# Optimization experiments

Hardware: AMD Instinct MI355X
Metric: run time of the kernel (lower is better)

The kernel has to match this reference:

```python
import jax, jax.numpy as jnp
import numpy as np

B, P, N, E, F, L = 64, 512, 512, 128, 512, 6
SQRT_E = 11.313708498984761
CLIP = 10.0
EPS = 1e-5

def _inorm(x, w, b):
    # InstanceNorm1d over node dim (axis=1) per (batch, channel); x: [B,N,E]
    mu = x.mean(axis=1, keepdims=True)
    var = x.var(axis=1, keepdims=True)
    return (x - mu) * jax.lax.rsqrt(var + EPS) * w + b

def setup_inputs():
    key = jax.random.key(0)
    ks = jax.random.split(key, 24)
    nrm = lambda k, shp, s=0.05: jax.random.normal(k, shp, dtype=jnp.float32) * s
    inp = {}
    inp['data'] = jax.random.uniform(ks[0], (B, N, 2), dtype=jnp.float32)
    inp['dist'] = -jax.random.uniform(ks[1], (B, N, N), dtype=jnp.float32)      # negative dist
    inp['cur_dist'] = -jax.random.uniform(ks[2], (B, P, N), dtype=jnp.float32)
    inp['capacity'] = jax.random.uniform(ks[3], (B, P), dtype=jnp.float32)
    inp['ninf_mask'] = jnp.zeros((B, P, N), jnp.float32)
    inp['log_scale'] = jnp.array([1.0], jnp.float32)
    # encoder params (Linear weights stored [in,out], i.e. torch weight transposed)
    inp['emb_W'] = nrm(ks[4], (2, E), 0.5); inp['emb_b'] = jnp.zeros((E,), jnp.float32)
    inp['Wq'] = nrm(ks[5], (L, E, E)); inp['Wk'] = nrm(ks[6], (L, E, E)); inp['Wv'] = nrm(ks[7], (L, E, E))
    inp['aft_alpha'] = jnp.ones((L,), jnp.float32)
    inp['n1_w'] = jnp.ones((L, E), jnp.float32); inp['n1_b'] = jnp.zeros((L, E), jnp.float32)
    inp['ff_W1'] = nrm(ks[8], (L, E, F)); inp['ff_b1'] = jnp.zeros((L, F), jnp.float32)
    inp['ff_W2'] = nrm(ks[9], (L, F, E)); inp['ff_b2'] = jnp.zeros((L, E), jnp.float32)
    inp['n2_w'] = jnp.ones((L, E), jnp.float32); inp['n2_b'] = jnp.zeros((L, E), jnp.float32)
    # decoder params
    inp['dWq'] = nrm(ks[10], (E + 1, E)); inp['dWk'] = nrm(ks[11], (E, E)); inp['dWv'] = nrm(ks[12], (E, E))
    inp['dec_aft_alpha'] = jnp.array([1.0], jnp.float32)
    inp['probs_alpha'] = jnp.array([1.0], jnp.float32)
    return inp

def reference(data, dist, cur_dist, capacity, ninf_mask, log_scale,
              emb_W, emb_b, Wq, Wk, Wv, aft_alpha, n1_w, n1_b,
              ff_W1, ff_b1, ff_W2, ff_b2, n2_w, n2_b,
              dWq, dWk, dWv, dec_aft_alpha, probs_alpha):
    ls = log_scale[0]
    # ---- encoder: stacked AFT layers ----
    x = data @ emb_W + emb_b                                   # [B,N,E]
    for l in range(L):
        q = x @ Wq[l]; k = x @ Wk[l]; v = x @ Wv[l]
        ad = jnp.exp(ls * aft_alpha[l] * dist)                 # [B,N,N]
        ek = jnp.exp(k)
        weighted = (ad @ (ek * v)) / (ad @ ek)                 # [B,N,E]
        out = jax.nn.sigmoid(q) * weighted
        h = _inorm(x + out, n1_w[l], n1_b[l])
        ff = jax.nn.relu(h @ ff_W1[l] + ff_b1[l]) @ ff_W2[l] + ff_b2[l]
        x = _inorm(h + ff, n2_w[l], n2_b[l])
    enc = x                                                    # [B,N,E]
    # ---- decoder ----
    k = enc @ dWk; v = enc @ dWv
    gmean = enc.mean(axis=1, keepdims=True)                    # [B,1,E]
    gmp = jnp.broadcast_to(gmean, (enc.shape[0], capacity.shape[1], enc.shape[2]))
    q = jnp.concatenate([gmp, capacity[:, :, None]], axis=2) @ dWq   # [B,P,E]
    ad = jnp.exp(ls * dec_aft_alpha[0] * cur_dist + ninf_mask)       # [B,P,N]
    ek = jnp.exp(k)
    weighted = (ad @ (ek * v)) / (ad @ ek)                     # [B,P,E]
    aft = jax.nn.sigmoid(q) * weighted
    score = jnp.einsum('bpe,bne->bpn', aft, enc) / SQRT_E
    score = score + ls * probs_alpha[0] * cur_dist
    score = CLIP * jnp.tanh(score) + ninf_mask
    return jax.nn.softmax(score, axis=2)                       # [B,P,N]
```

## Files before the change

### kernel.cpp

```cpp
#include <hip/hip_runtime.h>
#include <math.h>

#define B_ 64
#define N_ 512
#define P_ 512
#define E_ 128
#define F_ 512
#define L_ 6
#define SQRT_E_INV 0.08838834764831843f

typedef unsigned short u16;
typedef __attribute__((ext_vector_type(8))) short bf8;
typedef __attribute__((ext_vector_type(16))) float f16v;

__device__ inline u16 bf16r(float f) {
    unsigned u = __float_as_uint(f);
    u += 0x7fffu + ((u >> 16) & 1u);
    return (u16)(u >> 16);
}
__device__ inline float bf2f(u16 h) { return __uint_as_float((unsigned)h << 16); }

#define MFMA(a, b, c) __builtin_amdgcn_mfma_f32_32x32x16_bf16(a, b, c, 0, 0, 0)

struct Q3 {
    const u16 *A0, *A1;
    const u16 *qh, *ql, *vh, *vl, *kh, *kl;
    u16 *sq16, *y2t;
};

__launch_bounds__(256, 2) __global__ void qvk3_k(Q3 p)
{
    const int tid = threadIdx.x;
    const int lane = tid & 63, wv = tid >> 6;
    const int wm = wv & 1, wn = wv >> 1;
    const int ln = lane & 31, hk = lane >> 5;
    const int row0 = blockIdx.x * 64;

    __shared__ __align__(16) u16 As[2][64][40];
    __shared__ __align__(16) u16 Bs[6][128][40];

    f16v aq[2], av[2], ak[2];
#pragma unroll
    for (int nt = 0; nt < 2; ++nt)
#pragma unroll
        for (int q = 0; q < 16; ++q) { aq[nt][q] = 0.f; av[nt][q] = 0.f; ak[nt][q] = 0.f; }

    const int r = tid >> 2, kq = tid & 3;
    for (int k0 = 0; k0 < 128; k0 += 32) {
        size_t ga = (size_t)(row0 + r) * 128 + k0 + kq * 8;
        *(uint4*)&As[0][r][kq * 8] = *(const uint4*)(p.A0 + ga);
        *(uint4*)&As[1][r][kq * 8] = *(const uint4*)(p.A1 + ga);
#pragma unroll
        for (int i = 0; i < 2; ++i) {
            int s = tid + i * 256;
            int rb2 = s >> 2, q = s & 3;
            size_t gb = (size_t)rb2 * 128 + k0 + q * 8;
            *(uint4*)&Bs[0][rb2][q * 8] = *(const uint4*)(p.qh + gb);
            *(uint4*)&Bs[1][rb2][q * 8] = *(const uint4*)(p.ql + gb);
            *(uint4*)&Bs[2][rb2][q * 8] = *(const uint4*)(p.vh + gb);
            *(uint4*)&Bs[3][rb2][q * 8] = *(const uint4*)(p.vl + gb);
            *(uint4*)&Bs[4][rb2][q * 8] = *(const uint4*)(p.kh + gb);
            *(uint4*)&Bs[5][rb2][q * 8] = *(const uint4*)(p.kl + gb);
        }
        __syncthreads();
#pragma unroll
        for (int s = 0; s < 2; ++s) {
            bf8 ah = *(const bf8*)&As[0][wm * 32 + ln][s * 16 + hk * 8];
            bf8 al = *(const bf8*)&As[1][wm * 32 + ln][s * 16 + hk * 8];
#pragma unroll
            for (int nt = 0; nt < 2; ++nt) {
                const int br = wn * 64 + nt * 32 + ln, sc = s * 16 + hk * 8;
                bf8 bqh = *(const bf8*)&Bs[0][br][sc];
                bf8 bql = *(const bf8*)&Bs[1][br][sc];
                bf8 bvh = *(const bf8*)&Bs[2][br][sc];
                bf8 bvl = *(const bf8*)&Bs[3][br][sc];
                bf8 bkh = *(const bf8*)&Bs[4][br][sc];
                bf8 bkl = *(const bf8*)&Bs[5][br][sc];
                aq[nt] = MFMA(ah, bqh, aq[nt]);
                aq[nt] = MFMA(ah, bql, aq[nt]);
                aq[nt] = MFMA(al, bqh, aq[nt]);
                av[nt] = MFMA(ah, bvh, av[nt]);
                av[nt] = MFMA(ah, bvl, av[nt]);
                av[nt] = MFMA(al, bvh, av[nt]);
                ak[nt] = MFMA(ah, bkh, ak[nt]);
                ak[nt] = MFMA(ah, bkl, ak[nt]);
                ak[nt] = MFMA(al, bkh, ak[nt]);
            }
        }
        __syncthreads();
    }

#pragma unroll
    for (int nt = 0; nt < 2; ++nt) {
        int gn = wn * 64 + nt * 32 + ln;
#pragma unroll
        for (int g = 0; g < 4; ++g) {
            int rb = row0 + wm * 32 + g * 8 + hk * 4;
            int bb = rb >> 9, nb = rb & 511;
            u16 pe[4], pv[4];
#pragma unroll
            for (int rr = 0; rr < 4; ++rr) {
                float vq = aq[nt][g * 4 + rr];
                p.sq16[(size_t)(rb + rr) * 128 + gn] =
                    bf16r(1.f / (1.f + __expf(-vq)));
                u16 hv = bf16r(av[nt][g * 4 + rr]);
                u16 he = bf16r(__expf(ak[nt][g * 4 + rr]));
                pe[rr] = he;
                pv[rr] = bf16r(bf2f(hv) * bf2f(he));
            }
            uint2 ue, uv;
            ue.x = pe[0] | ((unsigned)pe[1] << 16);
            ue.y = pe[2] | ((unsigned)pe[3] << 16);
            uv.x = pv[0] | ((unsigned)pv[1] << 16);
            uv.y = pv[2] | ((unsigned)pv[3] << 16);
            *(uint2*)(p.y2t + (size_t)bb * 131072 + (size_t)gn * 512 + nb) = uv;
            *(uint2*)(p.y2t + (size_t)bb * 131072 + (size_t)(128 + gn) * 512 + nb) = ue;
        }
    }
}

struct QV {
    const u16 *A0, *A1;
    const u16 *vh, *vl, *kh, *kl;
    u16* y2t;
};

__launch_bounds__(256, 3) __global__ void qvk_vk_k(QV p)
{
    const int tid = threadIdx.x;
    const int lane = tid & 63, wv = tid >> 6;
    const int wm = wv & 1, wn = wv >> 1;
    const int ln = lane & 31, hk = lane >> 5;
    const int row0 = blockIdx.x * 64;

    __shared__ __align__(16) u16 As[2][64][40];
    __shared__ __align__(16) u16 Bs[4][128][40];

    f16v av[2], ak[2];
#pragma unroll
    for (int nt = 0; nt < 2; ++nt)
#pragma unroll
        for (int q = 0; q < 16; ++q) { av[nt][q] = 0.f; ak[nt][q] = 0.f; }

    const int r = tid >> 2, kq = tid & 3;
    for (int k0 = 0; k0 < 128; k0 += 32) {
        size_t ga = (size_t)(row0 + r) * 128 + k0 + kq * 8;
        *(uint4*)&As[0][r][kq * 8] = *(const uint4*)(p.A0 + ga);
        *(uint4*)&As[1][r][kq * 8] = *(const uint4*)(p.A1 + ga);
#pragma unroll
        for (int i = 0; i < 2; ++i) {
            int s = tid + i * 256;
            int rb2 = s >> 2, q = s & 3;
            size_t gb = (size_t)rb2 * 128 + k0 + q * 8;
            *(uint4*)&Bs[0][rb2][q * 8] = *(const uint4*)(p.vh + gb);
            *(uint4*)&Bs[1][rb2][q * 8] = *(const uint4*)(p.vl + gb);
            *(uint4*)&Bs[2][rb2][q * 8] = *(const uint4*)(p.kh + gb);
            *(uint4*)&Bs[3][rb2][q * 8] = *(const uint4*)(p.kl + gb);
        }
        __syncthreads();
#pragma unroll
        for (int s = 0; s < 2; ++s) {
            bf8 ah = *(const bf8*)&As[0][wm * 32 + ln][s * 16 + hk * 8];
            bf8 al = *(const bf8*)&As[1][wm * 32 + ln][s * 16 + hk * 8];
#pragma unroll
            for (int nt = 0; nt < 2; ++nt) {
                const int br = wn * 64 + nt * 32 + ln, sc = s * 16 + hk * 8;
                bf8 bvh = *(const bf8*)&Bs[0][br][sc];
                bf8 bvl = *(const bf8*)&Bs[1][br][sc];
                bf8 bkh = *(const bf8*)&Bs[2][br][sc];
                bf8 bkl = *(const bf8*)&Bs[3][br][sc];
                av[nt] = MFMA(ah, bvh, av[nt]);
                av[nt] = MFMA(ah, bvl, av[nt]);
                av[nt] = MFMA(al, bvh, av[nt]);
                ak[nt] = MFMA(ah, bkh, ak[nt]);
                ak[nt] = MFMA(ah, bkl, ak[nt]);
                ak[nt] = MFMA(al, bkh, ak[nt]);
            }
        }
        __syncthreads();
    }

#pragma unroll
    for (int nt = 0; nt < 2; ++nt) {
        int gn = wn * 64 + nt * 32 + ln;
#pragma unroll
        for (int g = 0; g < 4; ++g) {
            int rb = row0 + wm * 32 + g * 8 + hk * 4;
            int bb = rb >> 9, nb = rb & 511;
            u16 pe[4], pv[4];
#pragma unroll
            for (int rr = 0; rr < 4; ++rr) {
                u16 hv = bf16r(av[nt][g * 4 + rr]);
                u16 he = bf16r(__expf(ak[nt][g * 4 + rr]));
                pe[rr] = he;
                pv[rr] = bf16r(bf2f(hv) * bf2f(he));
            }
            uint2 ue, uv;
            ue.x = pe[0] | ((unsigned)pe[1] << 16);
            ue.y = pe[2] | ((unsigned)pe[3] << 16);
            uv.x = pv[0] | ((unsigned)pv[1] << 16);
            uv.y = pv[2] | ((unsigned)pv[3] << 16);
            *(uint2*)(p.y2t + (size_t)bb * 131072 + (size_t)gn * 512 + nb) = uv;
            *(uint2*)(p.y2t + (size_t)bb * 131072 + (size_t)(128 + gn) * 512 + nb) = ue;
        }
    }
}

struct AP2 {
    const u16 *A16;
    const u16 *B0, *sq;
    u16 *gh, *gl;
    const float *s1, *s2; int s2i;
};

template <int OPA, int SG>
__launch_bounds__(256, 3) __global__ void aft2_k(AP2 p)
{
    const int tid = threadIdx.x;
    const int lane = tid & 63, wv = tid >> 6;
    const int wm = wv & 1, wn = wv >> 1;
    const int ln = lane & 31, hk = lane >> 5;

    const int id = blockIdx.x;
    const int xcd = id & 7, slot = id >> 3;
    const int bz = xcd * 8 + (slot >> 3);
    const int row0 = (slot & 7) * 64;

    __shared__ __align__(16) u16 As[2][64][40];
    __shared__ __align__(16) u16 Bs[2][256][40];

    f16v acc[4];
#pragma unroll
    for (int j = 0; j < 4; ++j)
#pragma unroll
        for (int q = 0; q < 16; ++q) acc[j][q] = 0.f;

    const float ascale = (OPA == 1) ? p.s1[0] * p.s2[p.s2i] : 0.f;
    const u16* Af = p.A16 + (size_t)bz * 262144 + (size_t)row0 * 512;
    const u16* Bb = p.B0 + (size_t)bz * 131072;

    const int r = tid >> 2, kq = tid & 3;
    uint4 va;
    uint4 vb[4];

#define AFT_LOAD(K0)                                                          \
    {                                                                         \
        va = *(const uint4*)(Af + (size_t)r * 512 + (K0) + kq * 8);           \
        size_t gb = (size_t)tid * 512 + (K0);                                 \
        _Pragma("unroll") for (int q = 0; q < 4; ++q)                         \
            vb[q] = *(const uint4*)(Bb + gb + q * 8);                         \
    }

#define AFT_WRITE(BUF)                                                        \
    {                                                                         \
        u16 a8[8];                                                            \
        *(uint4*)a8 = va;                                                     \
        float f[8];                                                           \
        _Pragma("unroll") for (int j = 0; j < 8; ++j) {                       \
            float t = bf2f(a8[j]);                                            \
            if (OPA == 1) t *= ascale;                                        \
            f[j] = __expf(t);                                                 \
        }                                                                     \
        uint4 pk;                                                             \
        pk.x = bf16r(f[0]) | ((unsigned)bf16r(f[1]) << 16);                   \
        pk.y = bf16r(f[2]) | ((unsigned)bf16r(f[3]) << 16);                   \
        pk.z = bf16r(f[4]) | ((unsigned)bf16r(f[5]) << 16);                   \
        pk.w = bf16r(f[6]) | ((unsigned)bf16r(f[7]) << 16);                   \
        *(uint4*)&As[BUF][r][kq * 8] = pk;                                    \
        _Pragma("unroll") for (int q = 0; q < 4; ++q)                         \
            *(uint4*)&Bs[BUF][tid][q * 8] = vb[q];                            \
    }

#define AFT_COMPUTE(BUF)                                                      \
    {                                                                         \
        _Pragma("unroll") for (int s = 0; s < 2; ++s) {                       \
            bf8 ah = *(const bf8*)&As[BUF][wm * 32 + ln][s * 16 + hk * 8];    \
            _Pragma("unroll") for (int j = 0; j < 4; ++j) {                   \
                int br = ((j >> 1) << 7) + wn * 64 + ((j & 1) << 5) + ln;     \
                bf8 bh = *(const bf8*)&Bs[BUF][br][s * 16 + hk * 8];          \
                acc[j] = MFMA(ah, bh, acc[j]);                                \
            }                                                                 \
        }                                                                     \
    }

    AFT_LOAD(0);
    AFT_WRITE(0);
    __syncthreads();

    int cur = 0;
    for (int k0 = 32; k0 < 512; k0 += 32) {
        AFT_LOAD(k0);
        AFT_COMPUTE(cur);
        AFT_WRITE(cur ^ 1);
        __syncthreads();
        cur ^= 1;
    }
    AFT_COMPUTE(cur);

#undef AFT_LOAD
#undef AFT_WRITE
#undef AFT_COMPUTE

    const u16* sqb = SG ? (p.sq + (size_t)bz * 65536) : (const u16*)0;
    u16* ghb = p.gh + (size_t)bz * 65536;
    u16* glb = p.gl + (size_t)bz * 65536;
#pragma unroll
    for (int j = 0; j < 2; ++j) {
        int e = wn * 64 + j * 32 + ln;
#pragma unroll
        for (int g = 0; g < 4; ++g) {
#pragma unroll
            for (int rr = 0; rr < 4; ++rr) {
                int row = row0 + wm * 32 + g * 8 + hk * 4 + rr;
                float num = acc[j][g * 4 + rr];
                float den = acc[j + 2][g * 4 + rr];
                float pv = num / den;
                if (SG) pv *= bf2f(sqb[(size_t)row * 128 + e]);
                u16 hi = bf16r(pv);
                ghb[(size_t)row * 128 + e] = hi;
                glb[(size_t)row * 128 + e] = bf16r(pv - bf2f(hi));
            }
        }
    }
}

struct F12 {
    const u16 *A0, *A1;
    const u16 *w1h, *w1l;
    const u16 *w2h, *w2l;
    const float *b1, *b2;
    float* of;
};

__launch_bounds__(512, 2) __global__ void ffn12_k(F12 p)
{
    const int tid = threadIdx.x;
    const int lane = tid & 63, wv = tid >> 6;
    const int wm = wv & 1, wn = wv >> 1;
    const int ln = lane & 31, hk = lane >> 5;
    const int row0 = blockIdx.x * 64;

    __shared__ __align__(16) u16 Ws[2][2][128][72];
    __shared__ __align__(16) u16 ff1c[4][64][136];

    bf8 ar0[8], ar1[8];
    {
        const size_t arow = (size_t)(row0 + wm * 32 + ln) * 128;
#pragma unroll
        for (int s = 0; s < 8; ++s) {
            ar0[s] = *(const bf8*)(p.A0 + arow + s * 16 + hk * 8);
            ar1[s] = *(const bf8*)(p.A1 + arow + s * 16 + hk * 8);
        }
    }

    const int lcol = wn * 32 + ln;
    const int sc_ = tid >> 3, sq_ = tid & 7;
    uint4 wr[2][2];

#define F_LOAD1(CT, KC)                                                       \
    {                                                                         \
        _Pragma("unroll") for (int pl = 0; pl < 2; ++pl) {                    \
            const u16* src = pl ? p.w1l : p.w1h;                              \
            _Pragma("unroll") for (int it = 0; it < 2; ++it) {                \
                int c = sc_ + it * 64;                                        \
                wr[pl][it] = *(const uint4*)(src +                            \
                    (size_t)((CT) * 128 + c) * 128 + (KC) * 64 + sq_ * 8);    \
            }                                                                 \
        }                                                                     \
    }

#define F_LOAD2(J)                                                            \
    {                                                                         \
        _Pragma("unroll") for (int pl = 0; pl < 2; ++pl) {                    \
            const u16* src = pl ? p.w2l : p.w2h;                              \
            _Pragma("unroll") for (int it = 0; it < 2; ++it) {                \
                int c = sc_ + it * 64;                                        \
                wr[pl][it] = *(const uint4*)(src +                            \
                    (size_t)c * 512 + (J) * 64 + sq_ * 8);                    \
            }                                                                 \
        }                                                                     \
    }

#define F_STORE(BUF)                                                          \
    {                                                                         \
        _Pragma("unroll") for (int pl = 0; pl < 2; ++pl)                      \
            _Pragma("unroll") for (int it = 0; it < 2; ++it)                  \
                *(uint4*)&Ws[BUF][pl][sc_ + it * 64][sq_ * 8] = wr[pl][it];   \
    }

    F_LOAD1(0, 0);
    F_STORE(0);
    __syncthreads();
    int buf = 0;
    f16v a0, a1, a2;
#pragma unroll
    for (int st = 0; st < 8; ++st) {
        const int ct = st >> 1, kc = st & 1;
        if (st < 7) { F_LOAD1((st + 1) >> 1, (st + 1) & 1); }
        else        { F_LOAD2(0); }
        if (kc == 0) {
#pragma unroll
            for (int q = 0; q < 16; ++q) { a0[q] = 0.f; a1[q] = 0.f; a2[q] = 0.f; }
        }
#pragma unroll
        for (int s = 0; s < 4; ++s) {
            bf8 bh = *(const bf8*)&Ws[buf][0][lcol][s * 16 + hk * 8];
            bf8 bl = *(const bf8*)&Ws[buf][1][lcol][s * 16 + hk * 8];
            a0 = MFMA(ar0[kc * 4 + s], bh, a0);
            a1 = MFMA(ar0[kc * 4 + s], bl, a1);
            a2 = MFMA(ar1[kc * 4 + s], bh, a2);
        }
        if (kc == 1) {
            float bv = p.b1[ct * 128 + lcol];
#pragma unroll
            for (int g = 0; g < 4; ++g)
#pragma unroll
                for (int rr = 0; rr < 4; ++rr) {
                    int lr = wm * 32 + g * 8 + hk * 4 + rr;
                    float v = a0[g * 4 + rr] + a1[g * 4 + rr] + a2[g * 4 + rr] + bv;
                    ff1c[ct][lr][lcol] = bf16r(fmaxf(v, 0.f));
                }
        }
        F_STORE(buf ^ 1);
        __syncthreads();
        buf ^= 1;
    }

    f16v c0, c1;
#pragma unroll
    for (int q = 0; q < 16; ++q) { c0[q] = 0.f; c1[q] = 0.f; }
#pragma unroll
    for (int j = 0; j < 8; ++j) {
        if (j < 7) F_LOAD2(j + 1);
#pragma unroll
        for (int s = 0; s < 4; ++s) {
            bf8 af = *(const bf8*)&ff1c[j >> 1][wm * 32 + ln]
                                      [(j & 1) * 64 + s * 16 + hk * 8];
            bf8 bh = *(const bf8*)&Ws[buf][0][lcol][s * 16 + hk * 8];
            bf8 bl = *(const bf8*)&Ws[buf][1][lcol][s * 16 + hk * 8];
            c0 = MFMA(af, bh, c0);
            c1 = MFMA(af, bl, c1);
        }
        if (j < 7) {
            F_STORE(buf ^ 1);
            __syncthreads();
            buf ^= 1;
        }
    }

#undef F_LOAD1
#undef F_LOAD2
#undef F_STORE

    float bv = p.b2[lcol];
#pragma unroll
    for (int g = 0; g < 4; ++g)
#pragma unroll
        for (int rr = 0; rr < 4; ++rr) {
            int rb = row0 + wm * 32 + g * 8 + hk * 4 + rr;
            p.of[(size_t)rb * 128 + lcol] = c0[g * 4 + rr] + c1[g * 4 + rr] + bv;
        }
}

struct SP2 {
    const u16 *A0, *A1, *B0, *B1;
    float* out;
    const float *cd, *cm;
    const float *s1, *s2;
};

__launch_bounds__(512, 4) __global__ void score_sm_k(SP2 p)
{
    const int tid = threadIdx.x;
    const int lane = tid & 63, wv = tid >> 6;
    const int wm = wv & 1, wn = wv >> 1;
    const int ln = lane & 31, hk = lane >> 5;

    const int id = blockIdx.x;
    const int xcd = id & 7, s_ = id >> 3;
    const int bz = xcd * 8 + (s_ & 7);
    const int row0 = (s_ >> 3) * 64;

    __shared__ __align__(16) u16 As[2][64][136];
    __shared__ __align__(16) u16 Bs[2][128][72];
    __shared__ float rs[4][64];

#pragma unroll
    for (int i = 0; i < 4; ++i) {
        int idx = tid + i * 512;
        int pl = idx >> 10, rem = idx & 1023;
        int row = rem >> 4, q = rem & 15;
        const u16* src = pl ? p.A1 : p.A0;
        *(uint4*)&As[pl][row][q * 8] =
            *(const uint4*)(src + ((size_t)bz * 512 + row0 + row) * 128 + q * 8);
    }

    const float sp = p.s1[0] * p.s2[0];
    f16v accs[4];

#pragma unroll
    for (int ct = 0; ct < 4; ++ct) {
        const int gn = ct * 128 + wn * 32 + ln;
        float cdv[16], cmv[16];
#pragma unroll
        for (int g = 0; g < 4; ++g)
#pragma unroll
            for (int rr = 0; rr < 4; ++rr) {
                int grow = row0 + wm * 32 + g * 8 + hk * 4 + rr;
                size_t ix = (size_t)bz * 262144 + (size_t)grow * 512 + gn;
                cdv[g * 4 + rr] = p.cd[ix];
                cmv[g * 4 + rr] = p.cm[ix];
            }
#pragma unroll
        for (int q = 0; q < 16; ++q) accs[ct][q] = 0.f;

#pragma unroll
        for (int kh = 0; kh < 2; ++kh) {
            const int kc = kh * 64;
#pragma unroll
            for (int i = 0; i < 4; ++i) {
                int idx = tid + i * 512;
                int pl = idx >> 10, rem = idx & 1023;
                int row = rem >> 3, q = rem & 7;
                const u16* src = pl ? p.B1 : p.B0;
                *(uint4*)&Bs[pl][row][q * 8] =
                    *(const uint4*)(src + ((size_t)bz * 512 + ct * 128 + row) * 128
                                    + kc + q * 8);
            }
            __syncthreads();
#pragma unroll
            for (int s = 0; s < 4; ++s) {
                bf8 ah = *(const bf8*)&As[0][wm * 32 + ln][kc + s * 16 + hk * 8];
                bf8 al = *(const bf8*)&As[1][wm * 32 + ln][kc + s * 16 + hk * 8];
                bf8 bh = *(const bf8*)&Bs[0][wn * 32 + ln][s * 16 + hk * 8];
                bf8 bl = *(const bf8*)&Bs[1][wn * 32 + ln][s * 16 + hk * 8];
                accs[ct] = MFMA(ah, bh, accs[ct]);
                accs[ct] = MFMA(ah, bl, accs[ct]);
                accs[ct] = MFMA(al, bh, accs[ct]);
            }
            __syncthreads();
        }

#pragma unroll
        for (int i = 0; i < 16; ++i) {
            float sc = fmaf(accs[ct][i], SQRT_E_INV, sp * cdv[i]);
            float e2 = __expf(2.f * sc);
            float th = 1.f - 2.f / (e2 + 1.f);
            accs[ct][i] = __expf(10.f * th + cmv[i]);
        }
    }

    float rsum[16];
#pragma unroll
    for (int i = 0; i < 16; ++i)
        rsum[i] = accs[0][i] + accs[1][i] + accs[2][i] + accs[3][i];
#pragma unroll
    for (int i = 0; i < 16; ++i) {
#pragma unroll
        for (int o = 1; o < 32; o <<= 1) rsum[i] += __shfl_xor(rsum[i], o);
    }
    __syncthreads();
    if (ln == 0) {
#pragma unroll
        for (int i = 0; i < 16; ++i) {
            int lr = wm * 32 + (i >> 2) * 8 + hk * 4 + (i & 3);
            rs[wn][lr] = rsum[i];
        }
    }
    __syncthreads();
    float invr[16];
#pragma unroll
    for (int i = 0; i < 16; ++i) {
        int lr = wm * 32 + (i >> 2) * 8 + hk * 4 + (i & 3);
        invr[i] = 1.f / (rs[0][lr] + rs[1][lr] + rs[2][lr] + rs[3][lr]);
    }

#pragma unroll
    for (int ct = 0; ct < 4; ++ct) {
        int gn = ct * 128 + wn * 32 + ln;
#pragma unroll
        for (int g = 0; g < 4; ++g)
#pragma unroll
            for (int rr = 0; rr < 4; ++rr) {
                int grow = row0 + wm * 32 + g * 8 + hk * 4 + rr;
                size_t ix = (size_t)bz * 262144 + (size_t)grow * 512 + gn;
                p.out[ix] = accs[ct][g * 4 + rr] * invr[g * 4 + rr];
            }
    }
}

template <int MODE>
__launch_bounds__(256) __global__ void inorm_k(
    const u16* __restrict__ ah, const u16* __restrict__ al,
    const u16* __restrict__ g0, const u16* __restrict__ g1,
    const float* __restrict__ f1,
    const float* __restrict__ nw, const float* __restrict__ nbv,
    u16* __restrict__ oh, u16* __restrict__ ol)
{
    const int bb = blockIdx.x, e0 = blockIdx.y * 16;
    const int tid = threadIdx.x, el = tid & 3, no = tid >> 2;
    const size_t base = (size_t)bb * N_ * E_ + e0 + el * 4;

    float4 vals[8];
    float s1x = 0, s1y = 0, s1z = 0, s1w = 0;
    float s2x = 0, s2y = 0, s2z = 0, s2w = 0;
#pragma unroll
    for (int i = 0; i < 8; ++i) {
        int n = no * 8 + i;
        size_t ad = base + (size_t)n * E_;
        uint2 h2 = *(const uint2*)(ah + ad);
        uint2 l2 = *(const uint2*)(al + ad);
        float x0 = bf2f((u16)h2.x) + bf2f((u16)l2.x);
        float x1 = bf2f((u16)(h2.x >> 16)) + bf2f((u16)(l2.x >> 16));
        float x2 = bf2f((u16)h2.y) + bf2f((u16)l2.y);
        float x3 = bf2f((u16)(h2.y >> 16)) + bf2f((u16)(l2.y >> 16));
        float4 v;
        if (MODE == 1) {
            uint2 a2 = *(const uint2*)(g0 + ad);
            uint2 b2 = *(const uint2*)(g1 + ad);
            v.x = x0 + bf2f((u16)a2.x) + bf2f((u16)b2.x);
            v.y = x1 + bf2f((u16)(a2.x >> 16)) + bf2f((u16)(b2.x >> 16));
            v.z = x2 + bf2f((u16)a2.y) + bf2f((u16)b2.y);
            v.w = x3 + bf2f((u16)(a2.y >> 16)) + bf2f((u16)(b2.y >> 16));
        } else {
            float4 ff = *(const float4*)(f1 + ad);
            v.x = x0 + ff.x; v.y = x1 + ff.y; v.z = x2 + ff.z; v.w = x3 + ff.w;
        }
        vals[i] = v;
        s1x += v.x; s1y += v.y; s1z += v.z; s1w += v.w;
        s2x = fmaf(v.x, v.x, s2x); s2y = fmaf(v.y, v.y, s2y);
        s2z = fmaf(v.z, v.z, s2z); s2w = fmaf(v.w, v.w, s2w);
    }

    __shared__ float4 r1[256], r2[256];
    r1[tid] = make_float4(s1x, s1y, s1z, s1w);
    r2[tid] = make_float4(s2x, s2y, s2z, s2w);
    __syncthreads();
    for (int s = 128; s >= 4; s >>= 1) {
        if (tid < s) {
            float4 u = r1[tid], w = r1[tid + s];
            r1[tid] = make_float4(u.x + w.x, u.y + w.y, u.z + w.z, u.w + w.w);
            float4 pq = r2[tid], q = r2[tid + s];
            r2[tid] = make_float4(pq.x + q.x, pq.y + q.y, pq.z + q.z, pq.w + q.w);
        }
        __syncthreads();
    }
    __shared__ float4 mu_s[4], rs_s[4];
    if (tid < 4) {
        float4 m = r1[tid], q = r2[tid];
        m.x *= (1.f / N_); m.y *= (1.f / N_); m.z *= (1.f / N_); m.w *= (1.f / N_);
        q.x *= (1.f / N_); q.y *= (1.f / N_); q.z *= (1.f / N_); q.w *= (1.f / N_);
        float4 rsq;
        rsq.x = rsqrtf(q.x - m.x * m.x + 1e-5f);
        rsq.y = rsqrtf(q.y - m.y * m.y + 1e-5f);
        rsq.z = rsqrtf(q.z - m.z * m.z + 1e-5f);
        rsq.w = rsqrtf(q.w - m.w * m.w + 1e-5f);
        mu_s[tid] = m; rs_s[tid] = rsq;
    }
    __syncthreads();
    float4 mu = mu_s[el], rsq = rs_s[el];
    float4 w4 = *(const float4*)(nw + e0 + el * 4);
    float4 b4 = *(const float4*)(nbv + e0 + el * 4);
#pragma unroll
    for (int i = 0; i < 8; ++i) {
        size_t ad = base + (size_t)(no * 8 + i) * E_;
        float4 v = vals[i];
        v.x = fmaf((v.x - mu.x) * rsq.x, w4.x, b4.x);
        v.y = fmaf((v.y - mu.y) * rsq.y, w4.y, b4.y);
        v.z = fmaf((v.z - mu.z) * rsq.z, w4.z, b4.z);
        v.w = fmaf((v.w - mu.w) * rsq.w, w4.w, b4.w);
        u16 h0 = bf16r(v.x), h1 = bf16r(v.y), h2v = bf16r(v.z), h3 = bf16r(v.w);
        u16 l0 = bf16r(v.x - bf2f(h0)), l1 = bf16r(v.y - bf2f(h1));
        u16 l2v = bf16r(v.z - bf2f(h2v)), l3 = bf16r(v.w - bf2f(h3));
        uint2 ph, pl;
        ph.x = h0 | ((unsigned)h1 << 16); ph.y = h2v | ((unsigned)h3 << 16);
        pl.x = l0 | ((unsigned)l1 << 16); pl.y = l2v | ((unsigned)l3 << 16);
        *(uint2*)(oh + ad) = ph;
        *(uint2*)(ol + ad) = pl;
    }
}

__global__ void wprep_k(const float* __restrict__ W, u16* __restrict__ Th,
                        u16* __restrict__ Tl, int K, int N)
{
    const int z = blockIdx.z;
    const float* Wz = W + (size_t)z * K * N;
    u16* Hh = Th + (size_t)z * K * N;
    u16* Hl = Tl + (size_t)z * K * N;
    __shared__ float t[32][33];
    const int j = threadIdx.x & 31, i0 = threadIdx.x >> 5;
    const int k0 = blockIdx.x * 32, n0 = blockIdx.y * 32;
    for (int i = i0; i < 32; i += 8)
        t[i][j] = Wz[(size_t)(k0 + i) * N + n0 + j];
    __syncthreads();
    for (int i = i0; i < 32; i += 8) {
        float v = t[j][i];
        u16 h = bf16r(v);
        u16 l = bf16r(v - bf2f(h));
        size_t o = (size_t)(n0 + i) * K + k0 + j;
        Hh[o] = h; Hl[o] = l;
    }
}

__global__ void distprep_k(const float* __restrict__ src, u16* __restrict__ dst)
{
    size_t i = ((size_t)blockIdx.x * 256 + threadIdx.x) * 8;
    float4 f0 = *(const float4*)(src + i);
    float4 f1 = *(const float4*)(src + i + 4);
    uint4 pk;
    pk.x = bf16r(f0.x) | ((unsigned)bf16r(f0.y) << 16);
    pk.y = bf16r(f0.z) | ((unsigned)bf16r(f0.w) << 16);
    pk.z = bf16r(f1.x) | ((unsigned)bf16r(f1.y) << 16);
    pk.w = bf16r(f1.z) | ((unsigned)bf16r(f1.w) << 16);
    *(uint4*)(dst + i) = pk;
}

__global__ void decprep_k(const float* __restrict__ cd, const float* __restrict__ nf,
                          const float* __restrict__ s1, const float* __restrict__ s2,
                          u16* __restrict__ dst)
{
    const float da = s1[0] * s2[0];
    size_t i = ((size_t)blockIdx.x * 256 + threadIdx.x) * 8;
    float4 c0 = *(const float4*)(cd + i);
    float4 c1 = *(const float4*)(cd + i + 4);
    float4 m0 = *(const float4*)(nf + i);
    float4 m1 = *(const float4*)(nf + i + 4);
    uint4 pk;
    pk.x = bf16r(fmaf(da, c0.x, m0.x)) | ((unsigned)bf16r(fmaf(da, c0.y, m0.y)) << 16);
    pk.y = bf16r(fmaf(da, c0.z, m0.z)) | ((unsigned)bf16r(fmaf(da, c0.w, m0.w)) << 16);
    pk.z = bf16r(fmaf(da, c1.x, m1.x)) | ((unsigned)bf16r(fmaf(da, c1.y, m1.y)) << 16);
    pk.w = bf16r(fmaf(da, c1.z, m1.z)) | ((unsigned)bf16r(fmaf(da, c1.w, m1.w)) << 16);
    *(uint4*)(dst + i) = pk;
}

__global__ void embed_k(const float* __restrict__ data, const float* __restrict__ W,
                        const float* __restrict__ bias,
                        u16* __restrict__ xh, u16* __restrict__ xl)
{
    size_t idx = (size_t)blockIdx.x * 256 + threadIdx.x;
    int e = idx & 127;
    size_t bn = idx >> 7;
    float v = fmaf(data[bn * 2], W[e], fmaf(data[bn * 2 + 1], W[128 + e], bias[e]));
    u16 h = bf16r(v);
    xh[idx] = h;
    xl[idx] = bf16r(v - bf2f(h));
}

__launch_bounds__(512) __global__
void gq_k(const u16* __restrict__ xh, const u16* __restrict__ xl,
          const float* __restrict__ dWq, float* __restrict__ gq)
{
    int b = blockIdx.x;
    int tid = threadIdx.x;
    int e = tid & 127, qd = tid >> 7;
    float s = 0.f;
    for (int n = qd; n < N_; n += 4) {
        size_t ix = ((size_t)b * N_ + n) * E_ + e;
        s += bf2f(xh[ix]) + bf2f(xl[ix]);
    }
    __shared__ float part[512];
    __shared__ float gm[128];
    part[tid] = s;
    __syncthreads();
    if (tid < 128)
        gm[tid] = (part[tid] + part[tid + 128] + part[tid + 256] + part[tid + 384]) *
                  (1.f / N_);
    __syncthreads();
    if (tid < 128) {
        float acc = 0.f;
        for (int kk = 0; kk < 128; ++kk) acc = fmaf(gm[kk], dWq[kk * 128 + tid], acc);
        gq[b * 128 + tid] = acc;
    }
}

__global__ void dec_aft_k(const float* __restrict__ gq, const float* __restrict__ cap,
                          const float* __restrict__ dWq,
                          const u16* __restrict__ rh, const u16* __restrict__ rl,
                          u16* __restrict__ oh, u16* __restrict__ ol)
{
    size_t idx = (size_t)blockIdx.x * 256 + threadIdx.x;
    int e = idx & 127;
    size_t bp = idx >> 7;
    int b = (int)(bp >> 9);
    float q = fmaf(cap[bp], dWq[128 * 128 + e], gq[b * 128 + e]);
    float sg = 1.f / (1.f + __expf(-q));
    float v = sg * (bf2f(rh[idx]) + bf2f(rl[idx]));
    u16 h = bf16r(v);
    oh[idx] = h;
    ol[idx] = bf16r(v - bf2f(h));
}

extern "C" void kernel_launch(void* const* d_in, const int* in_sizes, int n_in,
                              void* d_out, int out_size, void* d_ws, size_t ws_size,
                              hipStream_t stream)
{
    const float* data      = (const float*)d_in[0];
    const float* dist      = (const float*)d_in[1];
    const float* cur_dist  = (const float*)d_in[2];
    const float* capacity  = (const float*)d_in[3];
    const float* ninf      = (const float*)d_in[4];
    const float* log_scale = (const float*)d_in[5];
    const float* emb_W     = (const float*)d_in[6];
    const float* emb_b     = (const float*)d_in[7];
    const float* Wq        = (const float*)d_in[8];
    const float* Wk        = (const float*)d_in[9];
    const float* Wv        = (const float*)d_in[10];
    const float* aft_alpha = (const float*)d_in[11];
    const float* n1_w      = (const float*)d_in[12];
    const float* n1_b      = (const float*)d_in[13];
    const float* ffW1      = (const float*)d_in[14];
    const float* ffb1      = (const float*)d_in[15];
    const float* ffW2      = (const float*)d_in[16];
    const float* ffb2      = (const float*)d_in[17];
    const float* n2_w      = (const float*)d_in[18];
    const float* n2_b      = (const float*)d_in[19];
    const float* dWq       = (const float*)d_in[20];
    const float* dWk       = (const float*)d_in[21];
    const float* dWv       = (const float*)d_in[22];
    const float* dec_alpha = (const float*)d_in[23];
    const float* p_alpha   = (const float*)d_in[24];
    float* out = (float*)d_out;

    char* W = (char*)d_ws;
    size_t off = 0;
    auto take = [&](size_t n) { void* pp = W + off; off += (n + 255) & ~(size_t)255; return pp; };
    const size_t SZP = (size_t)B_ * N_ * E_ * 2;

    u16* xh   = (u16*)take(SZP);
    u16* xl   = (u16*)take(SZP);
    u16* hh   = (u16*)take(SZP);
    u16* hl   = (u16*)take(SZP);
    u16* sq16 = (u16*)take(SZP);
    u16* gh   = (u16*)take(SZP);
    u16* gl   = (u16*)take(SZP);
    u16* y2t  = (u16*)take(2 * SZP);
    float* ff2 = (float*)take((size_t)B_ * N_ * E_ * 4);
    u16* d16  = (u16*)take((size_t)B_ * N_ * N_ * 2);
    u16* wqt_h = (u16*)take(196608); u16* wqt_l = (u16*)take(196608);
    u16* wkt_h = (u16*)take(196608); u16* wkt_l = (u16*)take(196608);
    u16* wvt_h = (u16*)take(196608); u16* wvt_l = (u16*)take(196608);
    u16* w1t_h = (u16*)take(786432); u16* w1t_l = (u16*)take(786432);
    u16* w2t_h = (u16*)take(786432); u16* w2t_l = (u16*)take(786432);
    u16* dkt_h = (u16*)take(32768);  u16* dkt_l = (u16*)take(32768);
    u16* dvt_h = (u16*)take(32768);  u16* dvt_l = (u16*)take(32768);
    float* gq = (float*)take(32768);
    if (ws_size < off) return;

    u16* am16 = d16;

    wprep_k<<<dim3(4, 4, 6), 256, 0, stream>>>(Wq, wqt_h, wqt_l, 128, 128);
    wprep_k<<<dim3(4, 4, 6), 256, 0, stream>>>(Wk, wkt_h, wkt_l, 128, 128);
    wprep_k<<<dim3(4, 4, 6), 256, 0, stream>>>(Wv, wvt_h, wvt_l, 128, 128);
    wprep_k<<<dim3(4, 16, 6), 256, 0, stream>>>(ffW1, w1t_h, w1t_l, 128, 512);
    wprep_k<<<dim3(16, 4, 6), 256, 0, stream>>>(ffW2, w2t_h, w2t_l, 512, 128);
    wprep_k<<<dim3(4, 4, 1), 256, 0, stream>>>(dWk, dkt_h, dkt_l, 128, 128);
    wprep_k<<<dim3(4, 4, 1), 256, 0, stream>>>(dWv, dvt_h, dvt_l, 128, 128);

    distprep_k<<<8192, 256, 0, stream>>>(dist, d16);
    embed_k<<<16384, 256, 0, stream>>>(data, emb_W, emb_b, xh, xl);

    for (int l = 0; l < L_; ++l) {
        Q3 q3{};
        q3.A0 = xh; q3.A1 = xl;
        q3.qh = wqt_h + l * 16384; q3.ql = wqt_l + l * 16384;
        q3.vh = wvt_h + l * 16384; q3.vl = wvt_l + l * 16384;
        q3.kh = wkt_h + l * 16384; q3.kl = wkt_l + l * 16384;
        q3.sq16 = sq16; q3.y2t = y2t;
        qvk3_k<<<512, 256, 0, stream>>>(q3);

        AP2 ap{};
        ap.A16 = d16; ap.B0 = y2t; ap.sq = sq16; ap.gh = gh; ap.gl = gl;
        ap.s1 = log_scale; ap.s2 = aft_alpha; ap.s2i = l;
        aft2_k<1, 1><<<512, 256, 0, stream>>>(ap);

        inorm_k<1><<<dim3(B_, 8), 256, 0, stream>>>(
            xh, xl, gh, gl, nullptr, n1_w + l * 128, n1_b + l * 128, hh, hl);

        F12 f12{};
        f12.A0 = hh; f12.A1 = hl;
        f12.w1h = w1t_h + l * 65536; f12.w1l = w1t_l + l * 65536;
        f12.w2h = w2t_h + l * 65536; f12.w2l = w2t_l + l * 65536;
        f12.b1 = ffb1 + l * 512; f12.b2 = ffb2 + l * 128;
        f12.of = ff2;
        ffn12_k<<<512, 512, 0, stream>>>(f12);

        inorm_k<2><<<dim3(B_, 8), 256, 0, stream>>>(
            hh, hl, nullptr, nullptr, ff2, n2_w + l * 128, n2_b + l * 128, xh, xl);
    }

    {
        QV qv{};
        qv.A0 = xh; qv.A1 = xl;
        qv.vh = dvt_h; qv.vl = dvt_l;
        qv.kh = dkt_h; qv.kl = dkt_l;
        qv.y2t = y2t;
        qvk_vk_k<<<512, 256, 0, stream>>>(qv);
        gq_k<<<B_, 512, 0, stream>>>(xh, xl, dWq, gq);

        decprep_k<<<8192, 256, 0, stream>>>(cur_dist, ninf, log_scale, dec_alpha, am16);

        AP2 ap{};
        ap.A16 = am16; ap.B0 = y2t; ap.gh = gh; ap.gl = gl;
        ap.s1 = log_scale; ap.s2 = dec_alpha; ap.s2i = 0;
        aft2_k<3, 0><<<512, 256, 0, stream>>>(ap);

        dec_aft_k<<<16384, 256, 0, stream>>>(gq, capacity, dWq, gh, gl, hh, hl);

        SP2 sp{};
        sp.A0 = hh; sp.A1 = hl; sp.B0 = xh; sp.B1 = xl;
        sp.out = out; sp.cd = cur_dist; sp.cm = ninf;
        sp.s1 = log_scale; sp.s2 = p_alpha;
        score_sm_k<<<512, 512, 0, stream>>>(sp);
    }
}
```

Baseline: 1.131 ms.

## Fuse decoder sigmoid gating into AFT epilogue and widen score kernel to 1024 threads

The separate dec_aft_k pass is removed. The sigmoid(q) gating is now computed inside the aft2_k epilogue (SG==2), which writes the hi/lo bf16 output directly and saves a full read/write round trip over the [B,P,E] intermediate. The score/softmax kernel is restructured to use 1024 threads. Each block now loads all 512 key rows per 32-wide K chunk and accumulates two 32x32 tiles per wave, instead of looping over four column tiles. This cuts the number of barrier/load phases, but it uses more LDS and registers per block and the launch-bound occupancy claim may not hold.

```diff
diff --git a/kernel.cpp b/kernel.cpp
--- a/kernel.cpp
+++ b/kernel.cpp
@@ -211,6 +211,7 @@
     const u16 *B0, *sq;
     u16 *gh, *gl;
     const float *s1, *s2; int s2i;
+    const float *gq, *cap, *dWq;
 };
 
 template <int OPA, int SG>
@@ -301,7 +302,7 @@
 #undef AFT_WRITE
 #undef AFT_COMPUTE
 
-    const u16* sqb = SG ? (p.sq + (size_t)bz * 65536) : (const u16*)0;
+    const u16* sqb = (SG == 1) ? (p.sq + (size_t)bz * 65536) : (const u16*)0;
     u16* ghb = p.gh + (size_t)bz * 65536;
     u16* glb = p.gl + (size_t)bz * 65536;
 #pragma unroll
@@ -315,7 +316,12 @@
                 float num = acc[j][g * 4 + rr];
                 float den = acc[j + 2][g * 4 + rr];
                 float pv = num / den;
-                if (SG) pv *= bf2f(sqb[(size_t)row * 128 + e]);
+                if (SG == 1) pv *= bf2f(sqb[(size_t)row * 128 + e]);
+                if (SG == 2) {
+                    float qv = fmaf(p.cap[(size_t)bz * 512 + row],
+                                    p.dWq[128 * 128 + e], p.gq[bz * 128 + e]);
+                    pv *= 1.f / (1.f + __expf(-qv));
+                }
                 u16 hi = bf16r(pv);
                 ghb[(size_t)row * 128 + e] = hi;
                 glb[(size_t)row * 128 + e] = bf16r(pv - bf2f(hi));
@@ -469,7 +475,7 @@
     const float *s1, *s2;
 };
 
-__launch_bounds__(512, 4) __global__ void score_sm_k(SP2 p)
+__launch_bounds__(1024, 4) __global__ void score_sm_k(SP2 p)
 {
     const int tid = threadIdx.x;
     const int lane = tid & 63, wv = tid >> 6;
@@ -482,12 +488,12 @@
     const int row0 = (s_ >> 3) * 64;
 
     __shared__ __align__(16) u16 As[2][64][136];
-    __shared__ __align__(16) u16 Bs[2][128][72];
-    __shared__ float rs[4][64];
-
-#pragma unroll
-    for (int i = 0; i < 4; ++i) {
-        int idx = tid + i * 512;
+    __shared__ __align__(16) u16 Bs[2][512][40];
+    __shared__ float rs[8][64];
+
+#pragma unroll
+    for (int i = 0; i < 2; ++i) {
+        int idx = tid + i * 1024;
         int pl = idx >> 10, rem = idx & 1023;
         int row = rem >> 4, q = rem & 15;
         const u16* src = pl ? p.A1 : p.A0;
@@ -496,11 +502,44 @@
     }
 
     const float sp = p.s1[0] * p.s2[0];
-    f16v accs[4];
-
-#pragma unroll
-    for (int ct = 0; ct < 4; ++ct) {
-        const int gn = ct * 128 + wn * 32 + ln;
+
+    f16v accs[2];
+#pragma unroll
+    for (int nt = 0; nt < 2; ++nt)
+#pragma unroll
+        for (int q = 0; q < 16; ++q) accs[nt][q] = 0.f;
+
+    for (int k0 = 0; k0 < 128; k0 += 32) {
+#pragma unroll
+        for (int i = 0; i < 4; ++i) {
+            int idx = tid + i * 1024;
+            int pl = idx >> 11, rem = idx & 2047;
+            int row = rem >> 2, q = rem & 3;
+            const u16* src = pl ? p.B1 : p.B0;
+            *(uint4*)&Bs[pl][row][q * 8] =
+                *(const uint4*)(src + ((size_t)bz * 512 + row) * 128 + k0 + q * 8);
+        }
+        __syncthreads();
+#pragma unroll
+        for (int s = 0; s < 2; ++s) {
+            bf8 ah = *(const bf8*)&As[0][wm * 32 + ln][k0 + s * 16 + hk * 8];
+            bf8 al = *(const bf8*)&As[1][wm * 32 + ln][k0 + s * 16 + hk * 8];
+#pragma unroll
+            for (int nt = 0; nt < 2; ++nt) {
+                bf8 bh = *(const bf8*)&Bs[0][wn * 64 + nt * 32 + ln][s * 16 + hk * 8];
+                bf8 bl = *(const bf8*)&Bs[1][wn * 64 + nt * 32 + ln][s * 16 + hk * 8];
+                accs[nt] = MFMA(ah, bh, accs[nt]);
+                accs[nt] = MFMA(ah, bl, accs[nt]);
+                accs[nt] = MFMA(al, bh, accs[nt]);
+            }
+        }
+        __syncthreads();
+    }
+
+    float rsum[16];
+#pragma unroll
+    for (int nt = 0; nt < 2; ++nt) {
+        const int gn = wn * 64 + nt * 32 + ln;
         float cdv[16], cmv[16];
 #pragma unroll
         for (int g = 0; g < 4; ++g)
@@ -512,48 +551,16 @@
                 cmv[g * 4 + rr] = p.cm[ix];
             }
 #pragma unroll
-        for (int q = 0; q < 16; ++q) accs[ct][q] = 0.f;
-
-#pragma unroll
-        for (int kh = 0; kh < 2; ++kh) {
-            const int kc = kh * 64;
-#pragma unroll
-            for (int i = 0; i < 4; ++i) {
-                int idx = tid + i * 512;
-                int pl = idx >> 10, rem = idx & 1023;
-                int row = rem >> 3, q = rem & 7;
-                const u16* src = pl ? p.B1 : p.B0;
-                *(uint4*)&Bs[pl][row][q * 8] =
-                    *(const uint4*)(src + ((size_t)bz * 512 + ct * 128 + row) * 128
-                                    + kc + q * 8);
-            }
-            __syncthreads();
-#pragma unroll
-            for (int s = 0; s < 4; ++s) {
-                bf8 ah = *(const bf8*)&As[0][wm * 32 + ln][kc + s * 16 + hk * 8];
-                bf8 al = *(const bf8*)&As[1][wm * 32 + ln][kc + s * 16 + hk * 8];
-                bf8 bh = *(const bf8*)&Bs[0][wn * 32 + ln][s * 16 + hk * 8];
-                bf8 bl = *(const bf8*)&Bs[1][wn * 32 + ln][s * 16 + hk * 8];
-                accs[ct] = MFMA(ah, bh, accs[ct]);
-                accs[ct] = MFMA(ah, bl, accs[ct]);
-                accs[ct] = MFMA(al, bh, accs[ct]);
-            }
-            __syncthreads();
-        }
-
-#pragma unroll
         for (int i = 0; i < 16; ++i) {
-            float sc = fmaf(accs[ct][i], SQRT_E_INV, sp * cdv[i]);
+            float sc = fmaf(accs[nt][i], SQRT_E_INV, sp * cdv[i]);
             float e2 = __expf(2.f * sc);
             float th = 1.f - 2.f / (e2 + 1.f);
-            accs[ct][i] = __expf(10.f * th + cmv[i]);
-        }
-    }
-
-    float rsum[16];
-#pragma unroll
-    for (int i = 0; i < 16; ++i)
-        rsum[i] = accs[0][i] + accs[1][i] + accs[2][i] + accs[3][i];
+            float ev = __expf(10.f * th + cmv[i]);
+            accs[nt][i] = ev;
+            if (nt == 0) rsum[i] = ev; else rsum[i] += ev;
+        }
+    }
+
 #pragma unroll
     for (int i = 0; i < 16; ++i) {
 #pragma unroll
@@ -572,19 +579,21 @@
 #pragma unroll
     for (int i = 0; i < 16; ++i) {
         int lr = wm * 32 + (i >> 2) * 8 + hk * 4 + (i & 3);
-        invr[i] = 1.f / (rs[0][lr] + rs[1][lr] + rs[2][lr] + rs[3][lr]);
-    }
-
-#pragma unroll
-    for (int ct = 0; ct < 4; ++ct) {
-        int gn = ct * 128 + wn * 32 + ln;
+        float t = rs[0][lr] + rs[1][lr] + rs[2][lr] + rs[3][lr]
+                + rs[4][lr] + rs[5][lr] + rs[6][lr] + rs[7][lr];
+        invr[i] = 1.f / t;
+    }
+
+#pragma unroll
+    for (int nt = 0; nt < 2; ++nt) {
+        int gn = wn * 64 + nt * 32 + ln;
 #pragma unroll
         for (int g = 0; g < 4; ++g)
 #pragma unroll
             for (int rr = 0; rr < 4; ++rr) {
                 int grow = row0 + wm * 32 + g * 8 + hk * 4 + rr;
                 size_t ix = (size_t)bz * 262144 + (size_t)grow * 512 + gn;
-                p.out[ix] = accs[ct][g * 4 + rr] * invr[g * 4 + rr];
+                p.out[ix] = accs[nt][g * 4 + rr] * invr[g * 4 + rr];
             }
     }
 }
@@ -771,23 +780,6 @@
         for (int kk = 0; kk < 128; ++kk) acc = fmaf(gm[kk], dWq[kk * 128 + tid], acc);
         gq[b * 128 + tid] = acc;
     }
-}
-
-__global__ void dec_aft_k(const float* __restrict__ gq, const float* __restrict__ cap,
-                          const float* __restrict__ dWq,
-                          const u16* __restrict__ rh, const u16* __restrict__ rl,
-                          u16* __restrict__ oh, u16* __restrict__ ol)
-{
-    size_t idx = (size_t)blockIdx.x * 256 + threadIdx.x;
-    int e = idx & 127;
-    size_t bp = idx >> 7;
-    int b = (int)(bp >> 9);
-    float q = fmaf(cap[bp], dWq[128 * 128 + e], gq[b * 128 + e]);
-    float sg = 1.f / (1.f + __expf(-q));
-    float v = sg * (bf2f(rh[idx]) + bf2f(rl[idx]));
-    u16 h = bf16r(v);
-    oh[idx] = h;
-    ol[idx] = bf16r(v - bf2f(h));
 }
 
 extern "C" void kernel_launch(void* const* d_in, const int* in_sizes, int n_in,
@@ -900,16 +892,15 @@
         decprep_k<<<8192, 256, 0, stream>>>(cur_dist, ninf, log_scale, dec_alpha, am16);
 
         AP2 ap{};
-        ap.A16 = am16; ap.B0 = y2t; ap.gh = gh; ap.gl = gl;
+        ap.A16 = am16; ap.B0 = y2t; ap.gh = hh; ap.gl = hl;
         ap.s1 = log_scale; ap.s2 = dec_alpha; ap.s2i = 0;
-        aft2_k<3, 0><<<512, 256, 0, stream>>>(ap);
-
-        dec_aft_k<<<16384, 256, 0, stream>>>(gq, capacity, dWq, gh, gl, hh, hl);
+        ap.gq = gq; ap.cap = capacity; ap.dWq = dWq;
+        aft2_k<3, 2><<<512, 256, 0, stream>>>(ap);
 
         SP2 sp{};
         sp.A0 = hh; sp.A1 = hl; sp.B0 = xh; sp.B1 = xl;
         sp.out = out; sp.cd = cur_dist; sp.cm = ninf;
         sp.s1 = log_scale; sp.s2 = p_alpha;
-        score_sm_k<<<512, 512, 0, stream>>>(sp);
-    }
-}
+        score_sm_k<<<512, 1024, 0, stream>>>(sp);
+    }
+}
```

After: 1.055 ms. 6.7% less time.
